# Performance work log

Measured on AMD Instinct MI355X. Metric: run time of the kernel, lower is better.

Reference implementation:

```python
import jax, jax.numpy as jnp
import numpy as np

EMBEDDING_DIM = 256
N_PITCHES = 128
N_VELOCITIES = 128
VOCAB_SIZE = 50257
N_CHORDS = 24
N_BEATS = 16
N_MELS = 128
N_GENRES = 10
N_TEMPOS = 10
N_KEYS = 12
N_MODES = 2
D_IN = EMBEDDING_DIM + N_PITCHES + N_VELOCITIES + VOCAB_SIZE + N_CHORDS + N_BEATS + N_MELS  # 50937
D_LYR = D_IN - EMBEDDING_DIM - N_PITCHES - N_VELOCITIES  # 50425
LENGTH = 16
T = LENGTH * N_PITCHES  # 2048 steps
EMB_VOCAB = N_GENRES + N_TEMPOS + N_KEYS + N_MODES + 1  # 35


def setup_inputs() -> dict:
    key = jax.random.key(0)
    ks = jax.random.split(key, 12)
    s = 1.0 / np.sqrt(D_IN).astype(np.float32)
    return dict(
        genre=jax.random.randint(ks[0], (1,), 0, N_GENRES, dtype=jnp.int64 if jax.config.jax_enable_x64 else jnp.int32),
        tempo=jax.random.randint(ks[1], (1,), 0, N_TEMPOS),
        key_sig=jax.random.randint(ks[2], (1,), 0, N_KEYS),
        length=LENGTH,
        melody_tensor=jax.random.normal(ks[3], (T, N_PITCHES + N_VELOCITIES), jnp.float32),
        lyrics_tensor=jax.random.normal(ks[4], (T, D_LYR), jnp.float32),
        emb=jax.random.normal(ks[5], (EMB_VOCAB, EMBEDDING_DIM), jnp.float32) * 0.02,
        conv_w=jax.random.normal(ks[6], (1, 1, 3, 3), jnp.float32) * (1.0 / 3.0),
        conv_b=jnp.zeros((1,), jnp.float32),
        w_chord=jax.random.normal(ks[7], (D_IN, N_CHORDS), jnp.float32) * s,
        b_chord=jnp.zeros((N_CHORDS,), jnp.float32),
        w_beat=jax.random.normal(ks[8], (D_IN, N_BEATS), jnp.float32) * s,
        b_beat=jnp.zeros((N_BEATS,), jnp.float32),
        w_mel=jax.random.normal(ks[9], (D_IN, N_MELS), jnp.float32) * s,
        b_mel=jnp.zeros((N_MELS,), jnp.float32),
    )


def reference(genre, tempo, key_sig, length, melody_tensor, lyrics_tensor,
              emb, conv_w, conv_b, w_chord, b_chord, w_beat, b_beat, w_mel, b_mel):
    # context ids: genre/tempo/key offset into the shared embedding table; last slot for the length token
    ids = jnp.concatenate([
        genre,
        tempo + N_GENRES,
        key_sig + N_GENRES + N_TEMPOS,
        jnp.array([EMB_VOCAB - 1], dtype=genre.dtype),
    ])
    ctx = emb[ids].sum(axis=0)  # [EMBEDDING_DIM]
    t = melody_tensor.shape[0]  # length * N_PITCHES steps, all batched
    # per-step 50937-dim feature vector: [context | melody pitch+vel | lyrics/state]
    x = jnp.concatenate([
        jnp.broadcast_to(ctx, (t, EMBEDDING_DIM)),
        melody_tensor,
        lyrics_tensor,
    ], axis=1)  # [T, D_IN]
    # 3x3 SAME conv on each step viewed as a 1x1xD_IN image (single in/out channel)
    xc = jax.lax.conv_general_dilated(
        x[:, None, None, :], conv_w,
        window_strides=(1, 1), padding=((1, 1), (1, 1)),
        dimension_numbers=('NCHW', 'OIHW', 'NCHW'))
    xc = xc[:, 0, 0, :] + conv_b[0]  # [T, D_IN]
    # three large-K linear heads, concatenated along features
    out = jnp.concatenate([
        xc @ w_chord + b_chord,
        xc @ w_beat + b_beat,
        xc @ w_mel + b_mel,
    ], axis=1)  # [T, N_CHORDS+N_BEATS+N_MELS] = [T, 168]
    return out
```

## Files before the change

kernel.cpp:

```cpp
#include <hip/hip_runtime.h>

#define D_IN_   50937
#define D_LYR_  50425
#define NCH     24
#define NBE     16
#define NME     128
#define NOUT    168
#define NPAD    192
#define KROWS   50688
#define KSPLIT  16
#define TOTSTEP 792
#define PARTN   (2048*168)

typedef __attribute__((ext_vector_type(8))) short short8;
typedef __attribute__((ext_vector_type(4))) float f32x4;
typedef float f32x4u __attribute__((ext_vector_type(4), aligned(4)));
typedef __attribute__((ext_vector_type(2))) unsigned int u32x2;
typedef __attribute__((address_space(3))) unsigned int lds_u32;
typedef const __attribute__((address_space(1))) unsigned int glob_u32;

static __device__ __forceinline__ unsigned short f2bf(float f) {
    unsigned int u = __float_as_uint(f);
    u += 0x7FFF + ((u >> 16) & 1);
    return (unsigned short)(u >> 16);
}
static __device__ __forceinline__ unsigned int pack2(float x, float y) {
    return (unsigned int)f2bf(x) | ((unsigned int)f2bf(y) << 16);
}

static __device__ __forceinline__ float wsrc(const float* wc, const float* wb,
                                             const float* wm, int d, int n) {
    if (n < NCH)        return wc[d * NCH + n];
    if (n < NCH + NBE)  return wb[d * NBE + (n - NCH)];
    if (n < NOUT)       return wm[(long)d * NME + (n - NCH - NBE)];
    return 0.f;
}
static __device__ __forceinline__ f32x4 wsrc4(const float* wc, const float* wb,
                                              const float* wm, int d, int nq) {
    int n0 = nq * 4;
    if (n0 < 24)  return *(const f32x4*)(wc + d * 24 + n0);
    if (n0 < 40)  return *(const f32x4*)(wb + d * 16 + (n0 - 24));
    if (n0 < 168) return *(const f32x4*)(wm + (long)d * 128 + (n0 - 40));
    f32x4 z = {0.f, 0.f, 0.f, 0.f};
    return z;
}

__global__ __launch_bounds__(256) void k_fold(const float* wc, const float* wb,
                                              const float* wm_, const float* conv_w,
                                              unsigned short* wbt) {
    __shared__ unsigned short tile[64 * 196];
    float cw0 = conv_w[3], cw1 = conv_w[4], cw2 = conv_w[5];
    int r0 = blockIdx.x * 64;
    int tid = threadIdx.x;
    for (int i = 0; i < 12; ++i) {
        int idx = tid + i * 256;
        int dl = idx / 48, nq = idx % 48;
        int r = r0 + dl;
        f32x4 v = {0.f, 0.f, 0.f, 0.f};
        if (r < 50681) {
            int d = 256 + r;
            f32x4 w0 = wsrc4(wc, wb, wm_, d, nq);
            f32x4 wn1 = wsrc4(wc, wb, wm_, d - 1, nq);
            v = cw1 * w0 + cw2 * wn1;
            if (d + 1 < D_IN_) v += cw0 * wsrc4(wc, wb, wm_, d + 1, nq);
        }
        u32x2 p; p.x = pack2(v.x, v.y); p.y = pack2(v.z, v.w);
        *(u32x2*)&tile[dl * 196 + nq * 4] = p;
    }
    __syncthreads();
    for (int i = 0; i < 6; ++i) {
        int idx = tid + i * 256;
        int n = idx >> 3, ch = idx & 7;
        short8 o;
        for (int j = 0; j < 8; ++j) o[j] = (short)tile[(ch * 8 + j) * 196 + n];
        *(short8*)(wbt + (long)n * KROWS + r0 + ch * 8) = o;
    }
}

__global__ void k_cvec(const int* genre, const int* tempo, const int* keysig,
                       const float* emb,
                       const float* wc, const float* wb, const float* wm_,
                       const float* conv_w, const float* conv_b,
                       const float* bc, const float* bb, const float* bm_, float* C) {
    int j = blockIdx.x;
    int lane = threadIdx.x;
    int g = genre[0], tt = tempo[0], kk = keysig[0];
    float cw0 = conv_w[3], cw1 = conv_w[4], cw2 = conv_w[5];
    float s = 0.f;
    for (int d = lane; d < 256; d += 64) {
        float cx = emb[g * 256 + d] + emb[(10 + tt) * 256 + d] +
                   emb[(20 + kk) * 256 + d] + emb[34 * 256 + d];
        float wp = cw1 * wsrc(wc, wb, wm_, d, j) + cw0 * wsrc(wc, wb, wm_, d + 1, j);
        if (d > 0) wp += cw2 * wsrc(wc, wb, wm_, d - 1, j);
        s += cx * wp;
    }
    float cb = conv_b[0];
    if (cb != 0.f) {
        float cs = 0.f;
        for (int d = lane; d < D_IN_; d += 64) cs += wsrc(wc, wb, wm_, d, j);
        s += cb * cs;
    }
    for (int off = 32; off; off >>= 1) s += __shfl_down(s, off);
    if (lane == 0) {
        float b = (j < NCH) ? bc[j] : (j < NCH + NBE) ? bb[j - NCH] : bm_[j - NCH - NBE];
        C[j] = s + b;
    }
}

__global__ __launch_bounds__(512, 4) void k_gemm(const float* mel, const float* lyr,
                                                 const unsigned short* wbt,
                                                 float* partial) {
    __shared__ unsigned short Bs[3 * NPAD * 64];
    const int blk = blockIdx.x;
    const int ks = ((blk & 7) << 1) | ((blk >> 3) & 1);
    const int bm = blk >> 4;
    const int tid = threadIdx.x, lane = tid & 63, wv = tid >> 6;
    const int wm = wv >> 1, wn = wv & 1;
    const int l15 = lane & 15, lk = lane >> 4;
    const int start = ks * 49 + (ks < 8 ? ks : 8);
    const int cnt = 49 + (ks < 8 ? 1 : 0);

    const int arow = bm * 64 + wm * 16 + l15;
    const float* melB = mel + arow * 256;
    const float* lyrB = lyr + (long)arow * D_LYR_ - 256;

    const int bnl = lane >> 3, bcs = lane & 7;

    f32x4 acc[6];
    #pragma unroll
    for (int i = 0; i < 6; ++i) acc[i] = (f32x4){0.f, 0.f, 0.f, 0.f};

    auto stageB = [&](int t, int buf) {
        int r0 = (start + t) * 64;
        #pragma unroll
        for (int j = 0; j < 3; ++j) {
            int n0 = wv * 24 + j * 8;
            int n = n0 + bnl;
            const unsigned short* gp =
                wbt + (long)n * KROWS + r0 + ((bcs ^ (n & 7)) * 8);
            __builtin_amdgcn_global_load_lds((glob_u32*)gp,
                                             (lds_u32*)(Bs + buf * (NPAD * 64) + n0 * 64),
                                             16, 0, 0);
        }
    };

    auto loadA = [&](int t, f32x4* dst) {
        int gt = start + t;
        int r0 = gt * 64;
        if (gt != TOTSTEP - 1) {
            #pragma unroll
            for (int kk = 0; kk < 2; ++kk) {
                int r = r0 + kk * 32 + lk * 8;
                const float* p = (r < 256) ? (melB + r) : (lyrB + r);
                dst[kk * 2]     = *(const f32x4u*)p;
                dst[kk * 2 + 1] = *(const f32x4u*)(p + 4);
            }
        } else {
            #pragma unroll
            for (int kk = 0; kk < 2; ++kk) {
                int r = r0 + kk * 32 + lk * 8;
                const float* p = lyrB + r;
                int c = r - 256;
                f32x4 v0, v1;
                #pragma unroll
                for (int q = 0; q < 4; ++q) {
                    v0[q] = (c + q     < D_LYR_) ? p[q]     : 0.f;
                    v1[q] = (c + 4 + q < D_LYR_) ? p[4 + q] : 0.f;
                }
                dst[kk * 2] = v0; dst[kk * 2 + 1] = v1;
            }
        }
    };

    auto compute = [&](const f32x4* a, int buf) {
        const unsigned short* Bb = Bs + buf * (NPAD * 64);
        #pragma unroll
        for (int kk = 0; kk < 2; ++kk) {
            f32x4 v0 = a[kk * 2], v1 = a[kk * 2 + 1];
            short8 af;
            af[0] = (short)f2bf(v0.x); af[1] = (short)f2bf(v0.y);
            af[2] = (short)f2bf(v0.z); af[3] = (short)f2bf(v0.w);
            af[4] = (short)f2bf(v1.x); af[5] = (short)f2bf(v1.y);
            af[6] = (short)f2bf(v1.z); af[7] = (short)f2bf(v1.w);
            #pragma unroll
            for (int ni = 0; ni < 6; ++ni) {
                int n = wn * 96 + ni * 16 + l15;
                int slot = (kk * 4 + lk) ^ (n & 7);
                short8 bf = *(const short8*)(Bb + n * 64 + slot * 8);
                acc[ni] = __builtin_amdgcn_mfma_f32_16x16x32_bf16(af, bf, acc[ni], 0, 0, 0);
            }
        }
    };

    f32x4 rg0[4], rg1[4], rg2[4];
    stageB(0, 0); loadA(0, rg0);
    stageB(1, 1); loadA(1, rg1);
    asm volatile("s_waitcnt vmcnt(11)" ::: "memory");
    __builtin_amdgcn_sched_barrier(0);
    __builtin_amdgcn_s_barrier();
    __builtin_amdgcn_sched_barrier(0);

#define PHASE(CUR, NXT, RGCUR, RGNXT)                                   \
    {                                                                   \
        bool pf = (t + 2 < cnt);                                        \
        if (pf) { stageB(t + 2, NXT); loadA(t + 2, RGNXT); }            \
        __builtin_amdgcn_sched_barrier(0);                              \
        compute(RGCUR, CUR);                                            \
        if (t + 1 >= cnt) break;                                        \
        if (pf) { asm volatile("s_waitcnt vmcnt(11)" ::: "memory"); }   \
        else    { asm volatile("s_waitcnt vmcnt(4)"  ::: "memory"); }   \
        __builtin_amdgcn_sched_barrier(0);                              \
        __builtin_amdgcn_s_barrier();                                   \
        __builtin_amdgcn_sched_barrier(0);                              \
        ++t;                                                            \
    }

    int t = 0;
    while (true) {
        PHASE(0, 2, rg0, rg2)
        PHASE(1, 0, rg1, rg0)
        PHASE(2, 1, rg2, rg1)
    }
#undef PHASE

    float* pbase = partial + (long)ks * PARTN;
    int rb = bm * 64 + wm * 16 + lk * 4;
    #pragma unroll
    for (int ni = 0; ni < 6; ++ni) {
        int col = wn * 96 + ni * 16 + l15;
        if (col < NOUT) {
            #pragma unroll
            for (int q = 0; q < 4; ++q)
                pbase[(long)(rb + q) * NOUT + col] = acc[ni][q];
        }
    }
}

__global__ void k_reduce(const float* partial, const float* C, float* out) {
    int idx = blockIdx.x * 256 + threadIdx.x;
    if (idx >= PARTN / 4) return;
    int base = idx * 4;
    f32x4 s;
    for (int q = 0; q < 4; ++q) s[q] = C[(base + q) % NOUT];
    for (int ks = 0; ks < KSPLIT; ++ks)
        s += *(const f32x4*)(partial + (long)ks * PARTN + base);
    *(f32x4*)(out + base) = s;
}

extern "C" void kernel_launch(void* const* d_in, const int* in_sizes, int n_in,
                              void* d_out, int out_size, void* d_ws, size_t ws_size,
                              hipStream_t stream) {
    const int*   genre   = (const int*)d_in[0];
    const int*   tempo   = (const int*)d_in[1];
    const int*   keysig  = (const int*)d_in[2];
    const float* mel     = (const float*)d_in[4];
    const float* lyr     = (const float*)d_in[5];
    const float* emb     = (const float*)d_in[6];
    const float* conv_w  = (const float*)d_in[7];
    const float* conv_b  = (const float*)d_in[8];
    const float* w_chord = (const float*)d_in[9];
    const float* b_chord = (const float*)d_in[10];
    const float* w_beat  = (const float*)d_in[11];
    const float* b_beat  = (const float*)d_in[12];
    const float* w_mel   = (const float*)d_in[13];
    const float* b_mel   = (const float*)d_in[14];

    char* ws = (char*)d_ws;
    unsigned short* wbt = (unsigned short*)ws;
    float* Cvec    = (float*)(ws + 19464192);
    float* partial = (float*)(ws + 19466240);
    float* out     = (float*)d_out;

    hipLaunchKernelGGL(k_fold, dim3(TOTSTEP), dim3(256), 0, stream,
                       w_chord, w_beat, w_mel, conv_w, wbt);
    hipLaunchKernelGGL(k_cvec, dim3(NOUT), dim3(64), 0, stream,
                       genre, tempo, keysig, emb,
                       w_chord, w_beat, w_mel, conv_w, conv_b,
                       b_chord, b_beat, b_mel, Cvec);
    hipLaunchKernelGGL(k_gemm, dim3(512), dim3(512), 0, stream,
                       mel, lyr, wbt, partial);
    hipLaunchKernelGGL(k_reduce, dim3((PARTN / 4 + 255) / 256), dim3(256), 0, stream,
                       partial, Cvec, out);
}
```

Baseline: 224.5 us.

## Stage B tiles through registers with double-buffered LDS instead of direct-to-LDS loads

```diff
diff --git a/kernel.cpp b/kernel.cpp
--- a/kernel.cpp
+++ b/kernel.cpp
@@ -16,8 +16,6 @@
 typedef __attribute__((ext_vector_type(4))) float f32x4;
 typedef float f32x4u __attribute__((ext_vector_type(4), aligned(4)));
 typedef __attribute__((ext_vector_type(2))) unsigned int u32x2;
-typedef __attribute__((address_space(3))) unsigned int lds_u32;
-typedef const __attribute__((address_space(1))) unsigned int glob_u32;
 
 static __device__ __forceinline__ unsigned short f2bf(float f) {
     unsigned int u = __float_as_uint(f);
@@ -110,7 +108,7 @@
 __global__ __launch_bounds__(512, 4) void k_gemm(const float* mel, const float* lyr,
                                                  const unsigned short* wbt,
                                                  float* partial) {
-    __shared__ unsigned short Bs[3 * NPAD * 64];
+    __shared__ unsigned short Bs[2 * NPAD * 64];
     const int blk = blockIdx.x;
     const int ks = ((blk & 7) << 1) | ((blk >> 3) & 1);
     const int bm = blk >> 4;
@@ -124,28 +122,31 @@
     const float* melB = mel + arow * 256;
     const float* lyrB = lyr + (long)arow * D_LYR_ - 256;
 
-    const int bnl = lane >> 3, bcs = lane & 7;
+    const int bn = tid >> 3, bch = tid & 7;
 
     f32x4 acc[6];
     #pragma unroll
     for (int i = 0; i < 6; ++i) acc[i] = (f32x4){0.f, 0.f, 0.f, 0.f};
 
-    auto stageB = [&](int t, int buf) {
-        int r0 = (start + t) * 64;
+    auto loadBreg = [&](int t2, short8* brg) {
+        int r0 = (start + t2) * 64;
         #pragma unroll
-        for (int j = 0; j < 3; ++j) {
-            int n0 = wv * 24 + j * 8;
-            int n = n0 + bnl;
-            const unsigned short* gp =
-                wbt + (long)n * KROWS + r0 + ((bcs ^ (n & 7)) * 8);
-            __builtin_amdgcn_global_load_lds((glob_u32*)gp,
-                                             (lds_u32*)(Bs + buf * (NPAD * 64) + n0 * 64),
-                                             16, 0, 0);
-        }
-    };
-
-    auto loadA = [&](int t, f32x4* dst) {
-        int gt = start + t;
+        for (int i = 0; i < 3; ++i) {
+            int n = bn + i * 64;
+            brg[i] = *(const short8*)(wbt + (long)n * KROWS + r0 + bch * 8);
+        }
+    };
+    auto writeB = [&](const short8* brg, int buf) {
+        char* Bb = (char*)Bs + buf * 24576;
+        #pragma unroll
+        for (int i = 0; i < 3; ++i) {
+            int n = bn + i * 64;
+            *(short8*)(Bb + n * 128 + ((bch * 16) ^ ((n & 7) << 4))) = brg[i];
+        }
+    };
+
+    auto loadA = [&](int t2, f32x4* dst) {
+        int gt = start + t2;
         int r0 = gt * 64;
         if (gt != TOTSTEP - 1) {
             #pragma unroll
@@ -173,7 +174,7 @@
     };
 
     auto compute = [&](const f32x4* a, int buf) {
-        const unsigned short* Bb = Bs + buf * (NPAD * 64);
+        const char* Bb = (const char*)Bs + buf * 24576;
         #pragma unroll
         for (int kk = 0; kk < 2; ++kk) {
             f32x4 v0 = a[kk * 2], v1 = a[kk * 2 + 1];
@@ -185,31 +186,35 @@
             #pragma unroll
             for (int ni = 0; ni < 6; ++ni) {
                 int n = wn * 96 + ni * 16 + l15;
-                int slot = (kk * 4 + lk) ^ (n & 7);
-                short8 bf = *(const short8*)(Bb + n * 64 + slot * 8);
+                int byte = n * 128 + (((kk * 64) + lk * 16) ^ ((n & 7) << 4));
+                short8 bf = *(const short8*)(Bb + byte);
                 acc[ni] = __builtin_amdgcn_mfma_f32_16x16x32_bf16(af, bf, acc[ni], 0, 0, 0);
             }
         }
     };
 
     f32x4 rg0[4], rg1[4], rg2[4];
-    stageB(0, 0); loadA(0, rg0);
-    stageB(1, 1); loadA(1, rg1);
-    asm volatile("s_waitcnt vmcnt(11)" ::: "memory");
-    __builtin_amdgcn_sched_barrier(0);
+    loadA(0, rg0);
+    loadA(1, rg1);
+    {
+        short8 b0[3];
+        loadBreg(0, b0);
+        writeB(b0, 0);
+    }
+    asm volatile("s_waitcnt lgkmcnt(0)" ::: "memory");
     __builtin_amdgcn_s_barrier();
     __builtin_amdgcn_sched_barrier(0);
 
-#define PHASE(CUR, NXT, RGCUR, RGNXT)                                   \
+#define PHASE(RGCUR, RGNXT, CURBUF)                                     \
     {                                                                   \
-        bool pf = (t + 2 < cnt);                                        \
-        if (pf) { stageB(t + 2, NXT); loadA(t + 2, RGNXT); }            \
-        __builtin_amdgcn_sched_barrier(0);                              \
-        compute(RGCUR, CUR);                                            \
-        if (t + 1 >= cnt) break;                                        \
-        if (pf) { asm volatile("s_waitcnt vmcnt(11)" ::: "memory"); }   \
-        else    { asm volatile("s_waitcnt vmcnt(4)"  ::: "memory"); }   \
-        __builtin_amdgcn_sched_barrier(0);                              \
+        if (t + 2 < cnt) loadA(t + 2, RGNXT);                           \
+        bool pfB = (t + 1 < cnt);                                       \
+        short8 brg[3];                                                  \
+        if (pfB) loadBreg(t + 1, brg);                                  \
+        compute(RGCUR, CURBUF);                                         \
+        if (!pfB) break;                                                \
+        writeB(brg, CURBUF ^ 1);                                        \
+        asm volatile("s_waitcnt lgkmcnt(0)" ::: "memory");              \
         __builtin_amdgcn_s_barrier();                                   \
         __builtin_amdgcn_sched_barrier(0);                              \
         ++t;                                                            \
@@ -217,9 +222,12 @@
 
     int t = 0;
     while (true) {
-        PHASE(0, 2, rg0, rg2)
-        PHASE(1, 0, rg1, rg0)
-        PHASE(2, 1, rg2, rg1)
+        PHASE(rg0, rg2, 0)
+        PHASE(rg1, rg0, 1)
+        PHASE(rg2, rg1, 0)
+        PHASE(rg0, rg2, 1)
+        PHASE(rg1, rg0, 0)
+        PHASE(rg2, rg1, 1)
     }
 #undef PHASE
 
```

Measured after the change: 456.9 us. 2.04x slower.
